# Kernel optimization log

Hardware: AMD Instinct MI355X
Metric: run time of the kernel (lower is better)

The kernel has to match this reference:

```python
import jax, jax.numpy as jnp
import numpy as np

B, N, O, H, A = 4096, 8, 64, 64, 16  # batch, agents, obs_dim, hx_size, actions
GH = 2 * H  # GRU input/hidden size = 128


def setup_inputs() -> dict:
    key = jax.random.key(0)
    ks = jax.random.split(key, 14)
    s = lambda *sh: 1.0 / np.sqrt(sh[-1])
    obs = jax.random.normal(ks[0], (B, N, O), dtype=jnp.float32)
    u = jax.random.uniform(ks[1], (B, N, N, 2), minval=1e-6, maxval=1.0 - 1e-6)
    gumbel = -jnp.log(-jnp.log(u))  # standard Gumbel noise, precomputed for determinism
    W1 = jax.random.normal(ks[2], (N, O, 128)) * s(O)
    b1 = jnp.zeros((N, 128), jnp.float32)
    W2 = jax.random.normal(ks[3], (N, 128, H)) * s(128)
    b2 = jnp.zeros((N, H), jnp.float32)
    # per ordered pair (i,j): single-step GRU cell, input GH, hidden GH
    Wi = jax.random.normal(ks[4], (N, N, 3 * GH, GH)) * s(GH)
    bi = jax.random.normal(ks[5], (N, N, 3 * GH)) * 0.01
    bh = jax.random.normal(ks[6], (N, N, 3 * GH)) * 0.01
    # gate head: GH -> 2 logits (G2ANet hard attention)
    Wg = jax.random.normal(ks[7], (N, N, 2, GH)) * s(GH)
    bg = jnp.zeros((N, N, 2), jnp.float32)
    # decode: concat(h_i, other_i) (2H) -> actions
    Wd = jax.random.normal(ks[8], (N, A, 2 * H)) * s(2 * H)
    bd = jnp.zeros((N, A), jnp.float32)
    return {"obs": obs, "gumbel": gumbel, "W1": W1, "b1": b1, "W2": W2, "b2": b2,
            "Wi": Wi, "bi": bi, "bh": bh, "Wg": Wg, "bg": bg, "Wd": Wd, "bd": bd}


def _forward(obs, gumbel, W1, b1, W2, b2, Wi, bi, bh, Wg, bg, Wd, bd):
    n = obs.shape[1]
    # per-agent encode MLP: [B,N,O] -> [B,N,H]
    h = jax.nn.relu(jnp.einsum('bno,noh->bnh', obs, W1) + b1)
    h = jax.nn.relu(jnp.einsum('bnh,nhk->bnk', h, W2) + b2)
    # pairwise input u[b,i,j] = concat(h_i, h_j)  -> [B,N,N,2H]
    bsz = h.shape[0]
    hi = jnp.broadcast_to(h[:, :, None, :], (bsz, n, n, H))
    hj = jnp.broadcast_to(h[:, None, :, :], (bsz, n, n, H))
    u = jnp.concatenate([hi, hj], axis=-1)
    # single-step GRU cell with zero initial hidden (Wh @ h0 == 0)
    gates = jnp.einsum('bijc,ijgc->bijg', u, Wi) + bi  # [B,N,N,3*GH]
    gr, gz, gn = jnp.split(gates, 3, axis=-1)
    br, bz, bn = jnp.split(bh, 3, axis=-1)
    r = jax.nn.sigmoid(gr + br)
    z = jax.nn.sigmoid(gz + bz)
    nn_ = jnp.tanh(gn + r * bn)
    g = (1.0 - z) * nn_  # GRU output, [B,N,N,GH]
    # 2-way gumbel-softmax, hard (straight-through)
    logits = jnp.einsum('bijc,ijoc->bijo', g, Wg) + bg  # [B,N,N,2]
    y_soft = jax.nn.softmax(logits + gumbel, axis=-1)  # tau = 1
    y_hard = jax.nn.one_hot(jnp.argmax(y_soft, axis=-1), 2, dtype=y_soft.dtype)
    y = jax.lax.stop_gradient(y_hard - y_soft) + y_soft
    w = y[..., 1] * (1.0 - jnp.eye(n, dtype=y.dtype))  # exclude self, [B,N,N]
    # gated aggregation of other agents' hiddens
    other = jnp.einsum('bij,bjh->bih', w, h)  # [B,N,H]
    comm = jnp.concatenate([h, other], axis=-1)  # [B,N,2H]
    q = jnp.einsum('bnc,nac->bna', comm, Wd) + bd  # [B,N,A]
    return q


def reference(obs, gumbel, W1, b1, W2, b2, Wi, bi, bh, Wg, bg, Wd, bd):
    return _forward(obs, gumbel, W1, b1, W2, b2, Wi, bi, bh, Wg, bg, Wd, bd)
```

## Files before the change

kernel.cpp:

```cpp
#include <hip/hip_runtime.h>

#define BATCH 4096
#define NAG   8
#define OBS   64
#define HD    64
#define GH    128
#define NACT  16
#define TAU   0.05f
#define CAP   65536

typedef short  bf16x8 __attribute__((ext_vector_type(8)));
typedef unsigned short u16x8 __attribute__((ext_vector_type(8)));
typedef float  f32x4  __attribute__((ext_vector_type(4)));

__device__ __forceinline__ float fast_sigmoid(float x) {
    return 1.f / (1.f + __expf(-x));
}
__device__ __forceinline__ float fast_tanh(float x) {
    x = fminf(fmaxf(x, -15.f), 15.f);
    const float e = __expf(2.f * x);
    return (e - 1.f) / (e + 1.f);
}
__device__ __forceinline__ unsigned short f2bf(float f) {
    unsigned int u = __builtin_bit_cast(unsigned int, f);
    u = (u + 0x7FFFu + ((u >> 16) & 1u)) >> 16;
    return (unsigned short)u;
}

__global__ void zero_counter(int* c) { if (threadIdx.x == 0) c[0] = 0; }

__global__ __launch_bounds__(256) void wiconv_kernel(
    const float* __restrict__ Wi, unsigned short* __restrict__ wib)
{
    const int t   = blockIdx.x * 256 + threadIdx.x;
    const int pp  = t / 6144;
    const int rem = t - pp * 6144;
    const int gp  = rem >> 4;
    const int k8  = rem & 15;
    const int pi  = pp / 7;
    int pj = pp % 7; pj += (pj >= pi);
    const int pb  = pi * NAG + pj;
    const int cg  = gp / 48;
    const int r2  = gp - cg * 48;
    const int s   = r2 >> 4, cl = r2 & 15;
    const int g   = s * GH + cg * 16 + cl;
    const float* src = Wi + ((size_t)pb * 384 + g) * GH + k8 * 8;
    u16x8 o;
#pragma unroll
    for (int e = 0; e < 8; ++e) o[e] = f2bf(src[e]);
    *reinterpret_cast<u16x8*>(wib + ((size_t)pb * 384 + gp) * GH + k8 * 8) = o;
}

__global__ __launch_bounds__(256, 2) void encode_kernel(
    const float* __restrict__ obs, const float* __restrict__ W1,
    const float* __restrict__ b1, const float* __restrict__ W2,
    const float* __restrict__ b2, float* __restrict__ h,
    unsigned short* __restrict__ hb)
{
    const int n    = blockIdx.x >> 6;
    const int tile = blockIdx.x & 63;
    const int b0   = tile * 64;
    const int tid  = threadIdx.x;

    __shared__ float u1[OBS * 68];
    __shared__ float h1t[GH * 68];
    __shared__ float wl[16 * GH];

    const float* __restrict__ W1n = W1 + n * (OBS * GH);
    const float* __restrict__ W2n = W2 + n * (GH * HD);
    const float* __restrict__ b1n = b1 + n * GH;
    const float* __restrict__ b2n = b2 + n * HD;

    {
        const int c  = tid & 63;
        const int r0 = tid >> 6;
        for (int rr = 0; rr < 16; ++rr) {
            const int bb = r0 * 16 + rr;
            u1[c * 68 + bb] = obs[((size_t)(b0 + bb) * NAG + n) * OBS + c];
        }
    }

    const int bq = tid & 15;
    const int cg = tid >> 4;

    float acc1[8][4];
#pragma unroll
    for (int cc = 0; cc < 8; ++cc)
#pragma unroll
        for (int bb = 0; bb < 4; ++bb) acc1[cc][bb] = 0.f;

    for (int kc = 0; kc < 4; ++kc) {
        __syncthreads();
#pragma unroll
        for (int p = 0; p < 2; ++p) {
            const int f = tid + p * 256;
            const int k = f >> 5, c4 = f & 31;
            *reinterpret_cast<float4*>(&wl[k * GH + c4 * 4]) =
                *reinterpret_cast<const float4*>(&W1n[(kc * 16 + k) * GH + c4 * 4]);
        }
        __syncthreads();
#pragma unroll 2
        for (int k = 0; k < 16; ++k) {
            const float4 uu = *reinterpret_cast<const float4*>(
                &u1[(kc * 16 + k) * 68 + bq * 4]);
            const float ub[4] = {uu.x, uu.y, uu.z, uu.w};
            const float4 wa = *reinterpret_cast<const float4*>(&wl[k * GH + cg * 8]);
            const float4 wb = *reinterpret_cast<const float4*>(&wl[k * GH + cg * 8 + 4]);
            const float wv[8] = {wa.x, wa.y, wa.z, wa.w, wb.x, wb.y, wb.z, wb.w};
#pragma unroll
            for (int cc = 0; cc < 8; ++cc)
#pragma unroll
                for (int bb = 0; bb < 4; ++bb)
                    acc1[cc][bb] += wv[cc] * ub[bb];
        }
    }

    {
        const float4 ba  = *reinterpret_cast<const float4*>(&b1n[cg * 8]);
        const float4 bb4 = *reinterpret_cast<const float4*>(&b1n[cg * 8 + 4]);
        const float bv[8] = {ba.x, ba.y, ba.z, ba.w, bb4.x, bb4.y, bb4.z, bb4.w};
#pragma unroll
        for (int cc = 0; cc < 8; ++cc)
#pragma unroll
            for (int bb = 0; bb < 4; ++bb)
                h1t[(cg * 8 + cc) * 68 + bq * 4 + bb] =
                    fmaxf(acc1[cc][bb] + bv[cc], 0.f);
    }

    const int og = tid >> 4;
    float acc2[4][4];
#pragma unroll
    for (int oc = 0; oc < 4; ++oc)
#pragma unroll
        for (int bb = 0; bb < 4; ++bb) acc2[oc][bb] = 0.f;

    for (int kc = 0; kc < 8; ++kc) {
        __syncthreads();
        {
            const int k = tid >> 4, o4 = tid & 15;
            *reinterpret_cast<float4*>(&wl[k * HD + o4 * 4]) =
                *reinterpret_cast<const float4*>(&W2n[(kc * 16 + k) * HD + o4 * 4]);
        }
        __syncthreads();
#pragma unroll 2
        for (int k = 0; k < 16; ++k) {
            const float4 uu = *reinterpret_cast<const float4*>(
                &h1t[(kc * 16 + k) * 68 + bq * 4]);
            const float ub[4] = {uu.x, uu.y, uu.z, uu.w};
            const float4 wa = *reinterpret_cast<const float4*>(&wl[k * HD + og * 4]);
            const float wv[4] = {wa.x, wa.y, wa.z, wa.w};
#pragma unroll
            for (int oc = 0; oc < 4; ++oc)
#pragma unroll
                for (int bb = 0; bb < 4; ++bb)
                    acc2[oc][bb] += wv[oc] * ub[bb];
        }
    }

    {
        const float4 b2v = *reinterpret_cast<const float4*>(&b2n[og * 4]);
#pragma unroll
        for (int bb = 0; bb < 4; ++bb) {
            float4 o;
            o.x = fmaxf(acc2[0][bb] + b2v.x, 0.f);
            o.y = fmaxf(acc2[1][bb] + b2v.y, 0.f);
            o.z = fmaxf(acc2[2][bb] + b2v.z, 0.f);
            o.w = fmaxf(acc2[3][bb] + b2v.w, 0.f);
            const size_t row = (size_t)(b0 + bq * 4 + bb) * NAG + n;
            *reinterpret_cast<float4*>(&h[row * HD + og * 4]) = o;
            ushort4 hv;
            hv.x = f2bf(o.x); hv.y = f2bf(o.y); hv.z = f2bf(o.z); hv.w = f2bf(o.w);
            *reinterpret_cast<ushort4*>(&hb[row * HD + og * 4]) = hv;
        }
    }
}

__global__ __launch_bounds__(256, 2) void pair_mfma_kernel(
    const unsigned short* __restrict__ hb, const unsigned short* __restrict__ wib,
    const float* __restrict__ bi, const float* __restrict__ bh,
    const float* __restrict__ Wg, const float* __restrict__ bg,
    const float* __restrict__ gum, float* __restrict__ wout,
    int* __restrict__ list, int* __restrict__ counter)
{
    const int pairp = blockIdx.x >> 6;
    const int tile  = blockIdx.x & 63;
    const int pi = pairp / 7;
    int pj = pairp % 7; pj += (pj >= pi);
    const int pb = pi * NAG + pj;
    const int b0 = tile * 64;

    const int tid = threadIdx.x;
    const int w   = tid >> 6;
    const int l   = tid & 63;
    const int cl  = l & 15;
    const int rg  = l >> 4;

    f32x4 acc[4][6];
#pragma unroll
    for (int bt = 0; bt < 4; ++bt)
#pragma unroll
        for (int t = 0; t < 6; ++t) acc[bt][t] = (f32x4){0.f, 0.f, 0.f, 0.f};

#pragma unroll
    for (int kb = 0; kb < 4; ++kb) {
        const int ag = (kb < 2) ? pi : pj;
        const int ch = (kb & 1) * 32 + rg * 8;
        bf16x8 av[4];
#pragma unroll
        for (int bt = 0; bt < 4; ++bt) {
            const int b = b0 + bt * 16 + cl;
            av[bt] = *reinterpret_cast<const bf16x8*>(
                &hb[((size_t)b * NAG + ag) * HD + ch]);
        }
        const size_t wbase = ((size_t)pb * 384 + w * 96 + cl) * GH + kb * 32 + rg * 8;
#pragma unroll
        for (int t = 0; t < 6; ++t) {
            const bf16x8 bv = *reinterpret_cast<const bf16x8*>(
                &wib[wbase + (size_t)t * 16 * GH]);
#pragma unroll
            for (int bt = 0; bt < 4; ++bt)
                acc[bt][t] = __builtin_amdgcn_mfma_f32_16x16x32_bf16(
                    av[bt], bv, acc[bt][t], 0, 0, 0);
        }
    }

    __shared__ float part[64][68];
    float pl[4][4];
#pragma unroll
    for (int bt = 0; bt < 4; ++bt)
#pragma unroll
        for (int r = 0; r < 4; ++r) pl[bt][r] = 0.f;

#pragma unroll
    for (int cgl = 0; cgl < 2; ++cgl) {
        const int c = (2 * w + cgl) * 16 + cl;
        const float bir = bi[pb * 384 + c];
        const float biz = bi[pb * 384 + 128 + c];
        const float bin = bi[pb * 384 + 256 + c];
        const float bhr = bh[pb * 384 + c];
        const float bhz = bh[pb * 384 + 128 + c];
        const float bhn = bh[pb * 384 + 256 + c];
        const float dwg = Wg[pb * 256 + 128 + c] - Wg[pb * 256 + c];
#pragma unroll
        for (int bt = 0; bt < 4; ++bt)
#pragma unroll
            for (int r = 0; r < 4; ++r) {
                const float rr = fast_sigmoid(acc[bt][cgl * 3 + 0][r] + bir + bhr);
                const float zz = fast_sigmoid(acc[bt][cgl * 3 + 1][r] + biz + bhz);
                const float nn = fast_tanh(acc[bt][cgl * 3 + 2][r] + bin + rr * bhn);
                pl[bt][r] += (1.f - zz) * nn * dwg;
            }
    }
#pragma unroll
    for (int bt = 0; bt < 4; ++bt)
#pragma unroll
        for (int r = 0; r < 4; ++r)
            part[bt * 16 + rg * 4 + r][w * 16 + cl] = pl[bt][r];
    __syncthreads();

    if (tid < 64) {
        float s = 0.f;
#pragma unroll
        for (int t = 0; t < 64; ++t) s += part[tid][t];
        const int b = b0 + tid;
        const float dbg = bg[pb * 2 + 1] - bg[pb * 2 + 0];
        const float* gp2 = gum + ((size_t)(b * NAG + pi) * NAG + pj) * 2;
        const float margin = s + dbg + (gp2[1] - gp2[0]);
        wout[(b * NAG + pi) * NAG + pj] = (margin > 0.f) ? 1.f : 0.f;
        if (fabsf(margin) < TAU) {
            const int idx = atomicAdd(counter, 1);
            if (idx < CAP) list[idx] = (b << 6) | (pi << 3) | pj;
        }
    }
}

__global__ __launch_bounds__(256) void refine_kernel(
    const float* __restrict__ h, const float* __restrict__ Wi,
    const float* __restrict__ bi, const float* __restrict__ bh,
    const float* __restrict__ Wg, const float* __restrict__ bg,
    const float* __restrict__ gum, const int* __restrict__ list,
    const int* __restrict__ counter, float* __restrict__ wout)
{
    __shared__ float u_sh[128];
    __shared__ float part[384 * 9];
    __shared__ float pl_sh[128];

    const int tid = threadIdx.x;
    const int rs  = tid >> 3;
    const int fs  = tid & 7;
    int count = counter[0]; if (count > CAP) count = CAP;

    for (int e = blockIdx.x; e < count; e += gridDim.x) {
        const int code = list[e];
        const int b = code >> 6, pi2 = (code >> 3) & 7, pj2 = code & 7;
        const int pb = pi2 * NAG + pj2;
        const float* __restrict__ Wr = Wi + (size_t)pb * 384 * GH;

        if (tid < 32) {
            const float* src = (tid < 16)
                ? h + ((size_t)b * NAG + pi2) * HD + tid * 4
                : h + ((size_t)b * NAG + pj2) * HD + (tid - 16) * 4;
            *reinterpret_cast<float4*>(&u_sh[tid * 4]) =
                *reinterpret_cast<const float4*>(src);
        }
        __syncthreads();

        float4 uv[4];
#pragma unroll
        for (int s = 0; s < 4; ++s)
            uv[s] = *reinterpret_cast<const float4*>(&u_sh[(fs + 8 * s) * 4]);

#pragma unroll 2
        for (int si = 0; si < 12; ++si) {
            const int r = si * 32 + rs;
            const float* row = Wr + (size_t)r * GH;
            float p = 0.f;
#pragma unroll
            for (int s = 0; s < 4; ++s) {
                const float4 wv = *reinterpret_cast<const float4*>(
                    row + (fs + 8 * s) * 4);
                p += wv.x * uv[s].x + wv.y * uv[s].y
                   + wv.z * uv[s].z + wv.w * uv[s].w;
            }
            part[r * 9 + fs] = p;
        }
        __syncthreads();

        if (tid < 128) {
            const int c = tid;
            float gr = 0.f, gz = 0.f, gn = 0.f;
#pragma unroll
            for (int k = 0; k < 8; ++k) {
                gr += part[c * 9 + k];
                gz += part[(128 + c) * 9 + k];
                gn += part[(256 + c) * 9 + k];
            }
            const float r = fast_sigmoid(gr + bi[pb*384 + c] + bh[pb*384 + c]);
            const float z = fast_sigmoid(gz + bi[pb*384 + 128 + c] + bh[pb*384 + 128 + c]);
            const float n = fast_tanh(gn + bi[pb*384 + 256 + c]
                                      + r * bh[pb*384 + 256 + c]);
            pl_sh[c] = (1.f - z) * n * (Wg[pb*256 + 128 + c] - Wg[pb*256 + c]);
        }
        __syncthreads();

        if (tid < 64) {
            float p = pl_sh[tid] + pl_sh[tid + 64];
#pragma unroll
            for (int m = 1; m < 64; m <<= 1) p += __shfl_xor(p, m, 64);
            if (tid == 0) {
                const float dbg = bg[pb * 2 + 1] - bg[pb * 2 + 0];
                const float* gp2 = gum + ((size_t)(b * NAG + pi2) * NAG + pj2) * 2;
                const float margin = p + dbg + (gp2[1] - gp2[0]);
                wout[(b * NAG + pi2) * NAG + pj2] = (margin > 0.f) ? 1.f : 0.f;
            }
        }
        __syncthreads();
    }
}

__global__ __launch_bounds__(256, 2) void agg_kernel(
    const float* __restrict__ h, const float* __restrict__ w,
    const float* __restrict__ Wd, const float* __restrict__ bd,
    float* __restrict__ q)
{
    const int b0 = blockIdx.x * 8;
    __shared__ float hl[8 * 520];
    const int tid = threadIdx.x;
#pragma unroll
    for (int p = 0; p < 4; ++p) {
        const int f = tid + p * 256;
        const int r = f >> 7, cc = (f & 127) * 4;
        *reinterpret_cast<float4*>(&hl[r * 520 + cc]) =
            *reinterpret_cast<const float4*>(&h[(size_t)b0 * 512 + f * 4]);
    }
    __syncthreads();

    const int aq = tid & 3;
    const int i  = (tid >> 2) & 7;
    const int bb = tid >> 5;
    const int b  = b0 + bb;

    float other[HD];
#pragma unroll
    for (int c = 0; c < HD; ++c) other[c] = 0.f;
    const float* wrow = w + ((size_t)b * NAG + i) * NAG;
    for (int j = 0; j < NAG; ++j) {
        if (j == i) continue;
        const float wv = wrow[j];
        const float* hr = &hl[bb * 520 + j * 64];
#pragma unroll
        for (int c4 = 0; c4 < HD / 4; ++c4) {
            const float4 v = *reinterpret_cast<const float4*>(hr + c4 * 4);
            other[c4*4+0] += wv * v.x; other[c4*4+1] += wv * v.y;
            other[c4*4+2] += wv * v.z; other[c4*4+3] += wv * v.w;
        }
    }
    const float* hi = &hl[bb * 520 + i * 64];
    const float* __restrict__ Wdp = Wd + (i * NACT) * (2 * HD);
    float qo[4];
#pragma unroll
    for (int t = 0; t < 4; ++t) {
        const int a = aq * 4 + t;
        float acc0 = bd[i * NACT + a];
        const float* wr = Wdp + a * 2 * HD;
#pragma unroll
        for (int c4 = 0; c4 < HD / 4; ++c4) {
            const float4 w1 = *reinterpret_cast<const float4*>(wr + c4 * 4);
            const float4 w2 = *reinterpret_cast<const float4*>(wr + 64 + c4 * 4);
            acc0 += hi[c4*4+0] * w1.x + hi[c4*4+1] * w1.y
                  + hi[c4*4+2] * w1.z + hi[c4*4+3] * w1.w
                  + other[c4*4+0] * w2.x + other[c4*4+1] * w2.y
                  + other[c4*4+2] * w2.z + other[c4*4+3] * w2.w;
        }
        qo[t] = acc0;
    }
    float4 qv = {qo[0], qo[1], qo[2], qo[3]};
    *reinterpret_cast<float4*>(&q[((size_t)b * NAG + i) * NACT + aq * 4]) = qv;
}

extern "C" void kernel_launch(void* const* d_in, const int* in_sizes, int n_in,
                              void* d_out, int out_size, void* d_ws, size_t ws_size,
                              hipStream_t stream) {
    const float* obs = (const float*)d_in[0];
    const float* gum = (const float*)d_in[1];
    const float* W1  = (const float*)d_in[2];
    const float* b1  = (const float*)d_in[3];
    const float* W2  = (const float*)d_in[4];
    const float* b2  = (const float*)d_in[5];
    const float* Wi  = (const float*)d_in[6];
    const float* bi  = (const float*)d_in[7];
    const float* bh  = (const float*)d_in[8];
    const float* Wg  = (const float*)d_in[9];
    const float* bg  = (const float*)d_in[10];
    const float* Wd  = (const float*)d_in[11];
    const float* bd  = (const float*)d_in[12];
    float* q = (float*)d_out;

    float*          ws   = (float*)d_ws;
    float*          h    = ws;
    float*          w    = ws + 2097152;
    unsigned short* hb   = (unsigned short*)(ws + 2359296);
    unsigned short* wib  = (unsigned short*)(ws + 3407872);
    int*            list = (int*)(ws + 4980736);
    int*            cnt  = (int*)(ws + 5046272);

    hipLaunchKernelGGL(zero_counter, dim3(1), dim3(64), 0, stream, cnt);
    hipLaunchKernelGGL(wiconv_kernel, dim3(1344), dim3(256), 0, stream, Wi, wib);
    hipLaunchKernelGGL(encode_kernel, dim3(NAG * (BATCH / 64)), dim3(256), 0, stream,
                       obs, W1, b1, W2, b2, h, hb);
    hipLaunchKernelGGL(pair_mfma_kernel, dim3(56 * 64), dim3(256), 0, stream,
                       hb, wib, bi, bh, Wg, bg, gum, w, list, cnt);
    hipLaunchKernelGGL(refine_kernel, dim3(2048), dim3(256), 0, stream,
                       h, Wi, bi, bh, Wg, bg, gum, list, cnt, w);
    hipLaunchKernelGGL(agg_kernel, dim3(BATCH / 8), dim3(256), 0, stream,
                       h, w, Wd, bd, q);
}
```

Baseline: 290.3 us.

## Split pair MFMA block across 8 waves, software-pipeline loads, precompute gate constants

```diff
diff --git a/kernel.cpp b/kernel.cpp
--- a/kernel.cpp
+++ b/kernel.cpp
@@ -6,8 +6,8 @@
 #define HD    64
 #define GH    128
 #define NACT  16
-#define TAU   0.05f
-#define CAP   65536
+#define TAU   0.025f
+#define CAP   16384
 
 typedef short  bf16x8 __attribute__((ext_vector_type(8)));
 typedef unsigned short u16x8 __attribute__((ext_vector_type(8)));
@@ -15,6 +15,9 @@
 
 __device__ __forceinline__ float fast_sigmoid(float x) {
     return 1.f / (1.f + __expf(-x));
+}
+__device__ __forceinline__ float sigmoid_negarg(float x) {
+    return 1.f / (1.f + __expf(x));
 }
 __device__ __forceinline__ float fast_tanh(float x) {
     x = fminf(fmaxf(x, -15.f), 15.f);
@@ -28,6 +31,22 @@
 }
 
 __global__ void zero_counter(int* c) { if (threadIdx.x == 0) c[0] = 0; }
+
+__global__ __launch_bounds__(128) void bprep_kernel(
+    const float* __restrict__ bi, const float* __restrict__ bh,
+    const float* __restrict__ Wg, float* __restrict__ econst)
+{
+    const int pp = blockIdx.x;
+    const int pi = pp / 7;
+    int pj = pp % 7; pj += (pj >= pi);
+    const int pb = pi * NAG + pj;
+    const int c  = threadIdx.x;
+    econst[0*8192 + pb*128 + c] = bi[pb*384 + c]       + bh[pb*384 + c];
+    econst[1*8192 + pb*128 + c] = bi[pb*384 + 128 + c] + bh[pb*384 + 128 + c];
+    econst[2*8192 + pb*128 + c] = bi[pb*384 + 256 + c];
+    econst[3*8192 + pb*128 + c] = bh[pb*384 + 256 + c];
+    econst[4*8192 + pb*128 + c] = Wg[pb*256 + 128 + c] - Wg[pb*256 + c];
+}
 
 __global__ __launch_bounds__(256) void wiconv_kernel(
     const float* __restrict__ Wi, unsigned short* __restrict__ wib)
@@ -175,10 +194,9 @@
     }
 }
 
-__global__ __launch_bounds__(256, 2) void pair_mfma_kernel(
+__global__ __launch_bounds__(512, 3) void pair_mfma_kernel(
     const unsigned short* __restrict__ hb, const unsigned short* __restrict__ wib,
-    const float* __restrict__ bi, const float* __restrict__ bh,
-    const float* __restrict__ Wg, const float* __restrict__ bg,
+    const float* __restrict__ econst, const float* __restrict__ bg,
     const float* __restrict__ gum, float* __restrict__ wout,
     int* __restrict__ list, int* __restrict__ counter)
 {
@@ -190,78 +208,103 @@
     const int b0 = tile * 64;
 
     const int tid = threadIdx.x;
-    const int w   = tid >> 6;
+    const int wv  = tid >> 6;
+    const int g   = wv & 3;
+    const int hh  = wv >> 2;
     const int l   = tid & 63;
     const int cl  = l & 15;
     const int rg  = l >> 4;
 
-    f32x4 acc[4][6];
-#pragma unroll
-    for (int bt = 0; bt < 4; ++bt)
-#pragma unroll
-        for (int t = 0; t < 6; ++t) acc[bt][t] = (f32x4){0.f, 0.f, 0.f, 0.f};
-
-#pragma unroll
-    for (int kb = 0; kb < 4; ++kb) {
-        const int ag = (kb < 2) ? pi : pj;
-        const int ch = (kb & 1) * 32 + rg * 8;
-        bf16x8 av[4];
-#pragma unroll
-        for (int bt = 0; bt < 4; ++bt) {
-            const int b = b0 + bt * 16 + cl;
-            av[bt] = *reinterpret_cast<const bf16x8*>(
-                &hb[((size_t)b * NAG + ag) * HD + ch]);
-        }
-        const size_t wbase = ((size_t)pb * 384 + w * 96 + cl) * GH + kb * 32 + rg * 8;
-#pragma unroll
-        for (int t = 0; t < 6; ++t) {
-            const bf16x8 bv = *reinterpret_cast<const bf16x8*>(
-                &wib[wbase + (size_t)t * 16 * GH]);
-#pragma unroll
-            for (int bt = 0; bt < 4; ++bt)
-                acc[bt][t] = __builtin_amdgcn_mfma_f32_16x16x32_bf16(
-                    av[bt], bv, acc[bt][t], 0, 0, 0);
-        }
-    }
-
-    __shared__ float part[64][68];
-    float pl[4][4];
-#pragma unroll
-    for (int bt = 0; bt < 4; ++bt)
-#pragma unroll
-        for (int r = 0; r < 4; ++r) pl[bt][r] = 0.f;
+    f32x4 acc[2][6];
+#pragma unroll
+    for (int bb = 0; bb < 2; ++bb)
+#pragma unroll
+        for (int t = 0; t < 6; ++t) acc[bb][t] = (f32x4){0.f, 0.f, 0.f, 0.f};
+
+    const size_t wbase = ((size_t)pb * 384 + g * 96 + cl) * GH + rg * 8;
+
+#define LOADA(dst, kb_) { \
+    const int ag = ((kb_) < 2) ? pi : pj; \
+    const int ch = ((kb_) & 1) * 32 + rg * 8; \
+    _Pragma("unroll") \
+    for (int bb = 0; bb < 2; ++bb) { \
+        const int b = b0 + (2 * hh + bb) * 16 + cl; \
+        dst[bb] = *reinterpret_cast<const bf16x8*>( \
+            &hb[((size_t)b * NAG + ag) * HD + ch]); } }
+
+#define LOADB(dst, kb_) { \
+    _Pragma("unroll") \
+    for (int t = 0; t < 6; ++t) \
+        dst[t] = *reinterpret_cast<const bf16x8*>( \
+            &wib[wbase + (size_t)(kb_) * 32 + (size_t)t * 16 * GH]); }
+
+#define MFMA6(a_, b_) { \
+    _Pragma("unroll") \
+    for (int t = 0; t < 6; ++t) \
+    _Pragma("unroll") \
+    for (int bb = 0; bb < 2; ++bb) \
+        acc[bb][t] = __builtin_amdgcn_mfma_f32_16x16x32_bf16( \
+            a_[bb], b_[t], acc[bb][t], 0, 0, 0); }
+
+    bf16x8 av0[2], av1[2], bv0[6], bv1[6];
+    LOADA(av0, 0); LOADB(bv0, 0);
+    LOADA(av1, 1); LOADB(bv1, 1);
+    MFMA6(av0, bv0);
+    LOADA(av0, 2); LOADB(bv0, 2);
+    MFMA6(av1, bv1);
+    LOADA(av1, 3); LOADB(bv1, 3);
+    MFMA6(av0, bv0);
+    MFMA6(av1, bv1);
+#undef LOADA
+#undef LOADB
+#undef MFMA6
+
+    __shared__ float part[64][69];
+    __shared__ float part2[64][9];
+    float pl[2][4];
+#pragma unroll
+    for (int bb = 0; bb < 2; ++bb)
+#pragma unroll
+        for (int r = 0; r < 4; ++r) pl[bb][r] = 0.f;
 
 #pragma unroll
     for (int cgl = 0; cgl < 2; ++cgl) {
-        const int c = (2 * w + cgl) * 16 + cl;
-        const float bir = bi[pb * 384 + c];
-        const float biz = bi[pb * 384 + 128 + c];
-        const float bin = bi[pb * 384 + 256 + c];
-        const float bhr = bh[pb * 384 + c];
-        const float bhz = bh[pb * 384 + 128 + c];
-        const float bhn = bh[pb * 384 + 256 + c];
-        const float dwg = Wg[pb * 256 + 128 + c] - Wg[pb * 256 + c];
-#pragma unroll
-        for (int bt = 0; bt < 4; ++bt)
+        const int c  = (2 * g + cgl) * 16 + cl;
+        const float br  = econst[0 * 8192 + pb * 128 + c];
+        const float bz  = econst[1 * 8192 + pb * 128 + c];
+        const float bn  = econst[2 * 8192 + pb * 128 + c];
+        const float bhn = econst[3 * 8192 + pb * 128 + c];
+        const float dw  = econst[4 * 8192 + pb * 128 + c];
+#pragma unroll
+        for (int bb = 0; bb < 2; ++bb)
 #pragma unroll
             for (int r = 0; r < 4; ++r) {
-                const float rr = fast_sigmoid(acc[bt][cgl * 3 + 0][r] + bir + bhr);
-                const float zz = fast_sigmoid(acc[bt][cgl * 3 + 1][r] + biz + bhz);
-                const float nn = fast_tanh(acc[bt][cgl * 3 + 2][r] + bin + rr * bhn);
-                pl[bt][r] += (1.f - zz) * nn * dwg;
+                const float rr  = fast_sigmoid(acc[bb][cgl * 3 + 0][r] + br);
+                const float omz = sigmoid_negarg(acc[bb][cgl * 3 + 1][r] + bz);
+                const float nn  = fast_tanh(acc[bb][cgl * 3 + 2][r] + bn + rr * bhn);
+                pl[bb][r] += omz * nn * dw;
             }
     }
 #pragma unroll
-    for (int bt = 0; bt < 4; ++bt)
+    for (int bb = 0; bb < 2; ++bb)
 #pragma unroll
         for (int r = 0; r < 4; ++r)
-            part[bt * 16 + rg * 4 + r][w * 16 + cl] = pl[bt][r];
+            part[g * 16 + cl][(2 * hh + bb) * 16 + rg * 4 + r] = pl[bb][r];
+    __syncthreads();
+
+    {
+        const int row = tid & 63, seg = tid >> 6;
+        float s = 0.f;
+#pragma unroll
+        for (int t = 0; t < 8; ++t) s += part[seg * 8 + t][row];
+        part2[row][seg] = s;
+    }
     __syncthreads();
 
     if (tid < 64) {
         float s = 0.f;
 #pragma unroll
-        for (int t = 0; t < 64; ++t) s += part[tid][t];
+        for (int t = 0; t < 8; ++t) s += part2[tid][t];
         const int b = b0 + tid;
         const float dbg = bg[pb * 2 + 1] - bg[pb * 2 + 0];
         const float* gp2 = gum + ((size_t)(b * NAG + pi) * NAG + pj) * 2;
@@ -436,20 +479,23 @@
     const float* bd  = (const float*)d_in[12];
     float* q = (float*)d_out;
 
-    float*          ws   = (float*)d_ws;
-    float*          h    = ws;
-    float*          w    = ws + 2097152;
-    unsigned short* hb   = (unsigned short*)(ws + 2359296);
-    unsigned short* wib  = (unsigned short*)(ws + 3407872);
-    int*            list = (int*)(ws + 4980736);
-    int*            cnt  = (int*)(ws + 5046272);
+    float*          ws     = (float*)d_ws;
+    float*          h      = ws;
+    float*          w      = ws + 2097152;
+    unsigned short* hb     = (unsigned short*)(ws + 2359296);
+    unsigned short* wib    = (unsigned short*)(ws + 3407872);
+    int*            list   = (int*)(ws + 4980736);
+    int*            cnt    = (int*)(ws + 4997120);
+    float*          econst = ws + 4997184;
 
     hipLaunchKernelGGL(zero_counter, dim3(1), dim3(64), 0, stream, cnt);
+    hipLaunchKernelGGL(bprep_kernel, dim3(56), dim3(128), 0, stream,
+                       bi, bh, Wg, econst);
     hipLaunchKernelGGL(wiconv_kernel, dim3(1344), dim3(256), 0, stream, Wi, wib);
     hipLaunchKernelGGL(encode_kernel, dim3(NAG * (BATCH / 64)), dim3(256), 0, stream,
                        obs, W1, b1, W2, b2, h, hb);
-    hipLaunchKernelGGL(pair_mfma_kernel, dim3(56 * 64), dim3(256), 0, stream,
-                       hb, wib, bi, bh, Wg, bg, gum, w, list, cnt);
+    hipLaunchKernelGGL(pair_mfma_kernel, dim3(56 * 64), dim3(512), 0, stream,
+                       hb, wib, econst, bg, gum, w, list, cnt);
     hipLaunchKernelGGL(refine_kernel, dim3(2048), dim3(256), 0, stream,
                        h, Wi, bi, bh, Wg, bg, gum, list, cnt, w);
     hipLaunchKernelGGL(agg_kernel, dim3(BATCH / 8), dim3(256), 0, stream,
```

Measured after the change: 293.7 us. No clear change (+1.2%).
